# Kernel optimization log

Measured on AMD Instinct MI355X. Metric: run time of the kernel, lower is better.

## Reference

```python
import jax, jax.numpy as jnp
import numpy as np

B, L, D = 4, 4096, 128
BLOCK, SPARSITY = 64, 0.9
NEG = -1e9


def _make_block_mask(key):
    nb = L // BLOCK
    bm = jax.random.uniform(key, (nb, nb)) > SPARSITY
    bm = bm | jnp.eye(nb, dtype=bool)  # keep diagonal blocks so no row is fully masked
    bm = jnp.tril(bm)
    return jnp.repeat(jnp.repeat(bm, BLOCK, axis=0), BLOCK, axis=1)  # [L, L]


def _xavier(key, shape):
    limit = float(np.sqrt(6.0 / (shape[0] + shape[1])))
    return jax.random.uniform(key, shape, jnp.float32, -limit, limit)


def setup_inputs() -> dict:
    key = jax.random.key(0)
    ks = jax.random.split(key, 10)
    t = lambda k: jax.random.normal(k, (B, L, D), jnp.float32)
    return {
        'q_real': t(ks[0]), 'q_imag': t(ks[1]),
        'k_real': t(ks[2]), 'k_imag': t(ks[3]),
        'v_real': t(ks[4]), 'v_imag': t(ks[5]),
        'W_qkv': _xavier(ks[6], (6 * D, 6 * D)),
        'b_qkv': jnp.zeros((6 * D,), jnp.float32),
        'W_out': _xavier(ks[7], (2 * D, 2 * D)),
        'b_out': jnp.zeros((2 * D,), jnp.float32),
        'block_mask': _make_block_mask(ks[8]),
    }


def reference(q_real, q_imag, k_real, k_imag, v_real, v_imag,
              W_qkv, b_qkv, W_out, b_out, block_mask):
    d = q_real.shape[-1]
    scale = d ** -0.5
    # fused qkv projection over the 6 concatenated channels
    x = jnp.concatenate([q_real, q_imag, k_real, k_imag, v_real, v_imag], axis=-1)  # [B,L,6D]
    qkv = (x @ W_qkv.T + b_qkv).reshape(x.shape[0], x.shape[1], 6, d)
    q_r, q_i, k_r, k_i, v_r, v_i = (qkv[:, :, j] for j in range(6))

    def attn(q, k, v):
        s = jnp.einsum('bqd,bkd->bqk', q, k) * scale          # [B,L,L]
        s = jnp.where(block_mask[None], s, NEG)               # block-sparse mask
        a = jax.nn.softmax(s, axis=-1)                        # dropout = identity (eval)
        return jnp.einsum('bqk,bkd->bqd', a, v)

    out = jnp.concatenate([attn(q_r, k_r, v_r), attn(q_i, k_i, v_i)], axis=-1)  # [B,L,2D]
    out = out @ W_out.T + b_out
    return out[..., :d], out[..., d:]
```

## Files before the change

kernel.cpp:

```cpp
#include <hip/hip_runtime.h>
#include <hip/hip_bf16.h>

typedef unsigned short u16;
typedef __attribute__((ext_vector_type(8))) short bf16x8;
typedef __attribute__((ext_vector_type(4))) float f32x4;

#define SEQ_L 4096
#define M_TOT 16384

__device__ __forceinline__ float bf2f(u16 x) {
    unsigned u = ((unsigned)x) << 16;
    return __builtin_bit_cast(float, u);
}
__device__ __forceinline__ u16 f2bf(float f) {
    unsigned u = __builtin_bit_cast(unsigned, f);
    u += 0x7FFFu + ((u >> 16) & 1u);
    return (u16)(u >> 16);
}
__device__ __forceinline__ void gload16(const u16* g, u16* l) {
    __builtin_amdgcn_global_load_lds(
        (const __attribute__((address_space(1))) unsigned int*)g,
        (__attribute__((address_space(3))) unsigned int*)l, 16, 0, 0);
}

__global__ __launch_bounds__(256) void prep_all(
    const float* __restrict__ in0, const float* __restrict__ in1, const float* __restrict__ in2,
    const float* __restrict__ in3, const float* __restrict__ in4, const float* __restrict__ in5,
    const float* __restrict__ Wqkv, const float* __restrict__ Wout, const void* __restrict__ mask,
    u16* __restrict__ x, u16* __restrict__ Wqkv_bf, u16* __restrict__ Wout_bf,
    unsigned char* __restrict__ cmask) {
    int id = blockIdx.x * 256 + threadIdx.x;
    if (id < 1572864) {
        const float* ins[6] = {in0, in1, in2, in3, in4, in5};
        int which = id >> 18, j = id & 262143;
        int m = j >> 4, c8 = j & 15;
        const float* sp = ins[which] + (size_t)m * 128 + c8 * 8;
        float4 a = *(const float4*)sp;
        float4 b = *(const float4*)(sp + 4);
        u16 t[8] = {f2bf(a.x), f2bf(a.y), f2bf(a.z), f2bf(a.w),
                    f2bf(b.x), f2bf(b.y), f2bf(b.z), f2bf(b.w)};
        *(uint4*)(x + (size_t)m * 768 + which * 128 + c8 * 8) = *(uint4*)t;
    } else if (id < 1572864 + 73728 + 8192) {
        int i = id - 1572864;
        const float* src = (i < 73728) ? Wqkv : Wout;
        u16* dst = (i < 73728) ? Wqkv_bf : Wout_bf;
        if (i >= 73728) i -= 73728;
        const float* sp = src + (size_t)i * 8;
        float4 a = *(const float4*)sp;
        float4 b = *(const float4*)(sp + 4);
        u16 t[8] = {f2bf(a.x), f2bf(a.y), f2bf(a.z), f2bf(a.w),
                    f2bf(b.x), f2bf(b.y), f2bf(b.z), f2bf(b.w)};
        *(uint4*)(dst + (size_t)i * 8) = *(uint4*)t;
    } else if (id < 1572864 + 73728 + 8192 + 4096) {
        int i = id - 1572864 - 73728 - 8192;
        int bi = i >> 6, bj = i & 63;
        size_t e = (size_t)(bi * 64) * SEQ_L + (size_t)bj * 64;
        const unsigned char* p8 = (const unsigned char*)mask;
        unsigned w0 = *(const unsigned*)mask;
        bool v;
        if (w0 == 0x01010101u || w0 == 0xFFFFFFFFu)      v = p8[e] != 0;
        else if (w0 == 0x3F803F80u || w0 == 0x3C003C00u) v = ((const u16*)mask)[e] != 0;
        else                                             v = ((const unsigned*)mask)[e] != 0;
        cmask[i] = v ? 1 : 0;
    }
}

__global__ __launch_bounds__(256, 4) void qkv_gemm(
    const u16* __restrict__ X, const u16* __restrict__ W, const float* __restrict__ bias,
    u16* __restrict__ qk, u16* __restrict__ vt) {
    __shared__ __align__(16) u16 As[128 * 64];
    __shared__ __align__(16) u16 Bs[64 * 64];
    int m0 = blockIdx.x * 128, n0 = blockIdx.y * 64;
    int tid = threadIdx.x, lane = tid & 63, w = tid >> 6;
    int ln = lane & 15, quad = lane >> 4;
    int rw = (w >> 1) * 64, cw = (w & 1) * 32;
    int lr8 = lane >> 3, lc = lane & 7;
    f32x4 acc[4][2] = {};
    for (int kk = 0; kk < 768; kk += 64) {
        __syncthreads();
        #pragma unroll
        for (int j = 0; j < 4; j++) {
            int r0 = w * 32 + j * 8, r = r0 + lr8;
            gload16(X + (size_t)(m0 + r) * 768 + kk + ((lc ^ (r & 7)) * 8), As + r0 * 64 + lane * 8);
        }
        #pragma unroll
        for (int j = 0; j < 2; j++) {
            int r0 = w * 16 + j * 8, r = r0 + lr8;
            gload16(W + (size_t)(n0 + r) * 768 + kk + ((lc ^ (r & 7)) * 8), Bs + r0 * 64 + lane * 8);
        }
        __syncthreads();
        #pragma unroll
        for (int s = 0; s < 2; s++) {
            bf16x8 af[4], bfr[2];
            #pragma unroll
            for (int i = 0; i < 4; i++) {
                int R = rw + i * 16 + ln;
                af[i] = *(const bf16x8*)(As + R * 64 + ((4 * s + quad) ^ (ln & 7)) * 8);
            }
            #pragma unroll
            for (int t = 0; t < 2; t++) {
                int R = cw + t * 16 + ln;
                bfr[t] = *(const bf16x8*)(Bs + R * 64 + ((4 * s + quad) ^ (ln & 7)) * 8);
            }
            #pragma unroll
            for (int i = 0; i < 4; i++)
                #pragma unroll
                for (int t = 0; t < 2; t++)
                    acc[i][t] = __builtin_amdgcn_mfma_f32_16x16x32_bf16(af[i], bfr[t], acc[i][t], 0, 0, 0);
        }
    }
    #pragma unroll
    for (int i = 0; i < 4; i++) {
        int row0 = m0 + rw + i * 16 + 4 * quad;
        #pragma unroll
        for (int t = 0; t < 2; t++) {
            int col = n0 + cw + t * 16 + ln;
            float bv = bias[col];
            if (col < 512) {
                #pragma unroll
                for (int r = 0; r < 4; r++)
                    qk[(size_t)(row0 + r) * 512 + col] = f2bf(acc[i][t][r] + bv);
            } else {
                int d = col - 512;
                int b = row0 >> 12, seq = row0 & 4095;
                u16 pk[4] = {f2bf(acc[i][t][0] + bv), f2bf(acc[i][t][1] + bv),
                             f2bf(acc[i][t][2] + bv), f2bf(acc[i][t][3] + bv)};
                *(ushort4*)(vt + ((size_t)(b * 2 + (d >> 7)) * 128 + (d & 127)) * SEQ_L + seq)
                    = *(ushort4*)pk;
            }
        }
    }
}

__global__ __launch_bounds__(256) void attn_out(
    const u16* __restrict__ qk, const u16* __restrict__ vt, const u16* __restrict__ Wout,
    const unsigned char* __restrict__ cmask, const float* __restrict__ bout,
    float* __restrict__ out) {
    __shared__ __align__(16) u16 Ks[2][64 * 128];
    __shared__ __align__(16) u16 Vt[2][128 * 64];
    __shared__ __align__(16) u16 PsAo[32 * 256];

    int idx = blockIdx.x;
    int qi = 63 - (idx >> 3);
    int b = (idx >> 1) & 3, half = idx & 1;
    int tid = threadIdx.x, lane = tid & 63, w = tid >> 6;
    int ln = lane & 15, quad = lane >> 4;
    int cw = w >> 1, wr = w & 1;
    const float scale = 0.08838834764831845f;

    const unsigned char* mrow = cmask + qi * 64;
    unsigned long long bm = 0;
    for (int k = 0; k <= qi; k++) bm |= (unsigned long long)(mrow[k] != 0) << k;

    const u16* kb_base = qk + (size_t)b * SEQ_L * 512 + 256 + cw * 128;
    const u16* vt_base = vt + (size_t)(b * 2 + cw) * 128 * SEQ_L;

    bf16x8 qf[4];
    {
        size_t grow = (size_t)(b * SEQ_L + qi * 64 + half * 32 + wr * 16 + ln);
        const u16* qp = qk + grow * 512 + cw * 128;
        #pragma unroll
        for (int s = 0; s < 4; s++) qf[s] = *(const bf16x8*)(qp + 32 * s + 8 * quad);
    }
    float m_st[4], l_st[4];
    #pragma unroll
    for (int r = 0; r < 4; r++) { m_st[r] = -1e30f; l_st[r] = 0.f; }
    f32x4 accO[8] = {};
    u16* Ps = PsAo + w * 1152;

    while (bm) {
        int cur = __ffsll(bm) - 1; bm &= bm - 1;
        __syncthreads();
        {
            const u16* kp = kb_base + (size_t)cur * 64 * 512;
            const u16* vp = vt_base + cur * 64;
            #pragma unroll
            for (int j = 0; j < 8; j++) {
                int kr0 = j * 8 + wr * 4, kr = kr0 + (lane >> 4);
                gload16(kp + (size_t)kr * 512 + (((lane & 15) ^ (kr & 7)) * 8),
                        Ks[cw] + kr0 * 128 + lane * 8);
                int d0 = j * 16 + wr * 8, d = d0 + (lane >> 3);
                gload16(vp + (size_t)d * SEQ_L + (((lane & 7) ^ (d & 7)) * 8),
                        Vt[cw] + d0 * 64 + lane * 8);
            }
        }
        __syncthreads();

        f32x4 accS[4] = {};
        #pragma unroll
        for (int s = 0; s < 4; s++) {
            #pragma unroll
            for (int t = 0; t < 4; t++) {
                int R = t * 16 + ln;
                bf16x8 bfr = *(const bf16x8*)(Ks[cw] + R * 128 + ((4 * s + quad) ^ (ln & 7)) * 8);
                accS[t] = __builtin_amdgcn_mfma_f32_16x16x32_bf16(qf[s], bfr, accS[t], 0, 0, 0);
            }
        }
        float P[4][4];
        #pragma unroll
        for (int r = 0; r < 4; r++) {
            float sv[4];
            float mx = -1e30f;
            #pragma unroll
            for (int t = 0; t < 4; t++) { sv[t] = accS[t][r] * scale; mx = fmaxf(mx, sv[t]); }
            #pragma unroll
            for (int off = 1; off < 16; off <<= 1) mx = fmaxf(mx, __shfl_xor(mx, off, 64));
            float nm = fmaxf(m_st[r], mx);
            float alpha = __expf(m_st[r] - nm);
            m_st[r] = nm;
            float rs = 0.f;
            #pragma unroll
            for (int t = 0; t < 4; t++) { float p = __expf(sv[t] - nm); P[t][r] = p; rs += p; }
            #pragma unroll
            for (int off = 1; off < 16; off <<= 1) rs += __shfl_xor(rs, off, 64);
            l_st[r] = l_st[r] * alpha + rs;
            #pragma unroll
            for (int nt = 0; nt < 8; nt++) accO[nt][r] *= alpha;
        }
        #pragma unroll
        for (int t = 0; t < 4; t++)
            #pragma unroll
            for (int r = 0; r < 4; r++)
                Ps[(4 * quad + r) * 72 + ln + 16 * t] = f2bf(P[t][r]);
        #pragma unroll
        for (int s2 = 0; s2 < 2; s2++) {
            bf16x8 pf = *(const bf16x8*)(Ps + ln * 72 + 32 * s2 + 8 * quad);
            #pragma unroll
            for (int nt = 0; nt < 8; nt++) {
                int R = nt * 16 + ln;
                bf16x8 vf = *(const bf16x8*)(Vt[cw] + R * 64 + ((4 * s2 + quad) ^ (ln & 7)) * 8);
                accO[nt] = __builtin_amdgcn_mfma_f32_16x16x32_bf16(pf, vf, accO[nt], 0, 0, 0);
            }
        }
    }

    __syncthreads();
    {
        float inv[4];
        #pragma unroll
        for (int r = 0; r < 4; r++) inv[r] = 1.0f / fmaxf(l_st[r], 1e-20f);
        #pragma unroll
        for (int nt = 0; nt < 8; nt++)
            #pragma unroll
            for (int r = 0; r < 4; r++)
                PsAo[(wr * 16 + 4 * quad + r) * 256 + cw * 128 + nt * 16 + ln]
                    = f2bf(accO[nt][r] * inv[r]);
    }

    u16* Bs = Ks[0];
    f32x4 oacc[2][4] = {};
    for (int kk = 0; kk < 4; kk++) {
        __syncthreads();
        #pragma unroll
        for (int j = 0; j < 8; j++) {
            int o0 = w * 64 + j * 8, o = o0 + (lane >> 3);
            gload16(Wout + (size_t)o * 256 + kk * 64 + (((lane & 7) ^ (o & 7)) * 8),
                    Bs + o0 * 64 + lane * 8);
        }
        __syncthreads();
        #pragma unroll
        for (int s = 0; s < 2; s++) {
            bf16x8 af[2], bfr[4];
            #pragma unroll
            for (int i = 0; i < 2; i++)
                af[i] = *(const bf16x8*)(PsAo + (i * 16 + ln) * 256 + kk * 64 + 32 * s + 8 * quad);
            #pragma unroll
            for (int t = 0; t < 4; t++) {
                int o = w * 64 + t * 16 + ln;
                bfr[t] = *(const bf16x8*)(Bs + o * 64 + ((4 * s + quad) ^ (ln & 7)) * 8);
            }
            #pragma unroll
            for (int i = 0; i < 2; i++)
                #pragma unroll
                for (int t = 0; t < 4; t++)
                    oacc[i][t] = __builtin_amdgcn_mfma_f32_16x16x32_bf16(af[i], bfr[t], oacc[i][t], 0, 0, 0);
        }
    }
    const size_t hlf = (size_t)M_TOT * 128;
    #pragma unroll
    for (int t = 0; t < 4; t++) {
        int o = w * 64 + t * 16 + ln;
        float bv = bout[o];
        float* base = (o < 128) ? (out + o) : (out + hlf + (o - 128));
        #pragma unroll
        for (int i = 0; i < 2; i++) {
            int row = b * SEQ_L + qi * 64 + half * 32 + i * 16 + 4 * quad;
            #pragma unroll
            for (int r = 0; r < 4; r++)
                base[(size_t)(row + r) * 128] = oacc[i][t][r] + bv;
        }
    }
}

extern "C" void kernel_launch(void* const* d_in, const int* in_sizes, int n_in,
                              void* d_out, int out_size, void* d_ws, size_t ws_size,
                              hipStream_t stream) {
    char* ws = (char*)d_ws;
    u16* x_bf    = (u16*)ws;
    u16* qk_buf  = x_bf + (size_t)M_TOT * 768;
    u16* vt_buf  = qk_buf + (size_t)M_TOT * 512;
    u16* Wqkv_bf = vt_buf + (size_t)1024 * SEQ_L;
    u16* Wout_bf = Wqkv_bf + 589824;
    unsigned char* cmask = (unsigned char*)(Wout_bf + 65536);

    hipLaunchKernelGGL(prep_all, dim3(6480), dim3(256), 0, stream,
                       (const float*)d_in[0], (const float*)d_in[1], (const float*)d_in[2],
                       (const float*)d_in[3], (const float*)d_in[4], (const float*)d_in[5],
                       (const float*)d_in[6], (const float*)d_in[8], d_in[10],
                       x_bf, Wqkv_bf, Wout_bf, cmask);
    hipLaunchKernelGGL(qkv_gemm, dim3(128, 12), dim3(256), 0, stream,
                       x_bf, Wqkv_bf, (const float*)d_in[7], qk_buf, vt_buf);
    hipLaunchKernelGGL(attn_out, dim3(512), dim3(256), 0, stream,
                       qk_buf, vt_buf, Wout_bf, cmask, (const float*)d_in[9], (float*)d_out);
}
```

Baseline: 219.7 us.

## Load K/V fragments directly into registers with software prefetch, drop LDS staging

```diff
diff --git a/kernel.cpp b/kernel.cpp
--- a/kernel.cpp
+++ b/kernel.cpp
@@ -132,13 +132,11 @@
     }
 }
 
-__global__ __launch_bounds__(256) void attn_out(
+__global__ __launch_bounds__(256, 2) void attn_out(
     const u16* __restrict__ qk, const u16* __restrict__ vt, const u16* __restrict__ Wout,
     const unsigned char* __restrict__ cmask, const float* __restrict__ bout,
     float* __restrict__ out) {
-    __shared__ __align__(16) u16 Ks[2][64 * 128];
-    __shared__ __align__(16) u16 Vt[2][128 * 64];
-    __shared__ __align__(16) u16 PsAo[32 * 256];
+    __shared__ __align__(16) u16 smem[24832];
 
     int idx = blockIdx.x;
     int qi = 63 - (idx >> 3);
@@ -152,8 +150,8 @@
     unsigned long long bm = 0;
     for (int k = 0; k <= qi; k++) bm |= (unsigned long long)(mrow[k] != 0) << k;
 
-    const u16* kb_base = qk + (size_t)b * SEQ_L * 512 + 256 + cw * 128;
-    const u16* vt_base = vt + (size_t)(b * 2 + cw) * 128 * SEQ_L;
+    const u16* kB = qk + (size_t)b * SEQ_L * 512 + 256 + cw * 128;
+    const u16* vB = vt + (size_t)(b * 2 + cw) * 128 * SEQ_L;
 
     bf16x8 qf[4];
     {
@@ -166,37 +164,44 @@
     #pragma unroll
     for (int r = 0; r < 4; r++) { m_st[r] = -1e30f; l_st[r] = 0.f; }
     f32x4 accO[8] = {};
-    u16* Ps = PsAo + w * 1152;
-
-    while (bm) {
-        int cur = __ffsll(bm) - 1; bm &= bm - 1;
-        __syncthreads();
-        {
-            const u16* kp = kb_base + (size_t)cur * 64 * 512;
-            const u16* vp = vt_base + cur * 64;
-            #pragma unroll
-            for (int j = 0; j < 8; j++) {
-                int kr0 = j * 8 + wr * 4, kr = kr0 + (lane >> 4);
-                gload16(kp + (size_t)kr * 512 + (((lane & 15) ^ (kr & 7)) * 8),
-                        Ks[cw] + kr0 * 128 + lane * 8);
-                int d0 = j * 16 + wr * 8, d = d0 + (lane >> 3);
-                gload16(vp + (size_t)d * SEQ_L + (((lane & 7) ^ (d & 7)) * 8),
-                        Vt[cw] + d0 * 64 + lane * 8);
-            }
-        }
-        __syncthreads();
-
+    u16* Ps = smem + w * 1152;
+
+    bf16x8 kf[4][4];
+    bf16x8 vf[8][2];
+    int cur = __ffsll(bm) - 1; bm &= bm - 1;
+    {
+        const u16* kp = kB + (size_t)cur * 64 * 512;
+        #pragma unroll
+        for (int t = 0; t < 4; t++)
+            #pragma unroll
+            for (int s = 0; s < 4; s++)
+                kf[t][s] = *(const bf16x8*)(kp + (size_t)(t * 16 + ln) * 512 + 32 * s + 8 * quad);
+        const u16* vp = vB + cur * 64;
+        #pragma unroll
+        for (int nt = 0; nt < 8; nt++)
+            #pragma unroll
+            for (int s2 = 0; s2 < 2; s2++)
+                vf[nt][s2] = *(const bf16x8*)(vp + (size_t)(nt * 16 + ln) * SEQ_L + 32 * s2 + 8 * quad);
+    }
+    while (cur >= 0) {
         f32x4 accS[4] = {};
         #pragma unroll
-        for (int s = 0; s < 4; s++) {
-            #pragma unroll
-            for (int t = 0; t < 4; t++) {
-                int R = t * 16 + ln;
-                bf16x8 bfr = *(const bf16x8*)(Ks[cw] + R * 128 + ((4 * s + quad) ^ (ln & 7)) * 8);
-                accS[t] = __builtin_amdgcn_mfma_f32_16x16x32_bf16(qf[s], bfr, accS[t], 0, 0, 0);
-            }
-        }
-        float P[4][4];
+        for (int s = 0; s < 4; s++)
+            #pragma unroll
+            for (int t = 0; t < 4; t++)
+                accS[t] = __builtin_amdgcn_mfma_f32_16x16x32_bf16(qf[s], kf[t][s], accS[t], 0, 0, 0);
+
+        int nxt = -1;
+        if (bm) { nxt = __ffsll(bm) - 1; bm &= bm - 1; }
+        if (nxt >= 0) {
+            const u16* kp = kB + (size_t)nxt * 64 * 512;
+            #pragma unroll
+            for (int t = 0; t < 4; t++)
+                #pragma unroll
+                for (int s = 0; s < 4; s++)
+                    kf[t][s] = *(const bf16x8*)(kp + (size_t)(t * 16 + ln) * 512 + 32 * s + 8 * quad);
+        }
+
         #pragma unroll
         for (int r = 0; r < 4; r++) {
             float sv[4];
@@ -210,7 +215,11 @@
             m_st[r] = nm;
             float rs = 0.f;
             #pragma unroll
-            for (int t = 0; t < 4; t++) { float p = __expf(sv[t] - nm); P[t][r] = p; rs += p; }
+            for (int t = 0; t < 4; t++) {
+                float p = __expf(sv[t] - nm);
+                Ps[(4 * quad + r) * 72 + ln + 16 * t] = f2bf(p);
+                rs += p;
+            }
             #pragma unroll
             for (int off = 1; off < 16; off <<= 1) rs += __shfl_xor(rs, off, 64);
             l_st[r] = l_st[r] * alpha + rs;
@@ -218,23 +227,26 @@
             for (int nt = 0; nt < 8; nt++) accO[nt][r] *= alpha;
         }
         #pragma unroll
-        for (int t = 0; t < 4; t++)
-            #pragma unroll
-            for (int r = 0; r < 4; r++)
-                Ps[(4 * quad + r) * 72 + ln + 16 * t] = f2bf(P[t][r]);
-        #pragma unroll
         for (int s2 = 0; s2 < 2; s2++) {
             bf16x8 pf = *(const bf16x8*)(Ps + ln * 72 + 32 * s2 + 8 * quad);
             #pragma unroll
-            for (int nt = 0; nt < 8; nt++) {
-                int R = nt * 16 + ln;
-                bf16x8 vf = *(const bf16x8*)(Vt[cw] + R * 64 + ((4 * s2 + quad) ^ (ln & 7)) * 8);
-                accO[nt] = __builtin_amdgcn_mfma_f32_16x16x32_bf16(pf, vf, accO[nt], 0, 0, 0);
-            }
-        }
+            for (int nt = 0; nt < 8; nt++)
+                accO[nt] = __builtin_amdgcn_mfma_f32_16x16x32_bf16(pf, vf[nt][s2], accO[nt], 0, 0, 0);
+        }
+        if (nxt >= 0) {
+            const u16* vp = vB + nxt * 64;
+            #pragma unroll
+            for (int nt = 0; nt < 8; nt++)
+                #pragma unroll
+                for (int s2 = 0; s2 < 2; s2++)
+                    vf[nt][s2] = *(const bf16x8*)(vp + (size_t)(nt * 16 + ln) * SEQ_L + 32 * s2 + 8 * quad);
+        }
+        cur = nxt;
     }
 
     __syncthreads();
+    u16* Ao = smem;
+    u16* Bs = smem + 32 * 264;
     {
         float inv[4];
         #pragma unroll
@@ -243,11 +255,10 @@
         for (int nt = 0; nt < 8; nt++)
             #pragma unroll
             for (int r = 0; r < 4; r++)
-                PsAo[(wr * 16 + 4 * quad + r) * 256 + cw * 128 + nt * 16 + ln]
+                Ao[(wr * 16 + 4 * quad + r) * 264 + cw * 128 + nt * 16 + ln]
                     = f2bf(accO[nt][r] * inv[r]);
     }
 
-    u16* Bs = Ks[0];
     f32x4 oacc[2][4] = {};
     for (int kk = 0; kk < 4; kk++) {
         __syncthreads();
@@ -263,7 +274,7 @@
             bf16x8 af[2], bfr[4];
             #pragma unroll
             for (int i = 0; i < 2; i++)
-                af[i] = *(const bf16x8*)(PsAo + (i * 16 + ln) * 256 + kk * 64 + 32 * s + 8 * quad);
+                af[i] = *(const bf16x8*)(Ao + (i * 16 + ln) * 264 + kk * 64 + 32 * s + 8 * quad);
             #pragma unroll
             for (int t = 0; t < 4; t++) {
                 int o = w * 64 + t * 16 + ln;
```

Result: slower. 248.2 us (+13.0%).
